# Kernel tuning notes

Hardware: AMD Instinct MI355X
Metric: run time of the kernel (lower is better)

Reference implementation:

```python
import jax, jax.numpy as jnp
import numpy as np

D_IN = 1024
D_OUT = 1024
NUM_HEAD = 16
HEAD_DIM = D_OUT // NUM_HEAD
CTX = 2048


def setup_inputs() -> dict:
    key = jax.random.key(0)
    ks = jax.random.split(key, 7)
    s = 0.02
    x = jax.random.normal(ks[0], (2, CTX, D_IN), dtype=jnp.float32)
    Wq = jax.random.normal(ks[1], (D_IN, D_OUT), dtype=jnp.float32) * s
    Wk = jax.random.normal(ks[2], (D_IN, D_OUT), dtype=jnp.float32) * s
    Wv = jax.random.normal(ks[3], (D_IN, D_OUT), dtype=jnp.float32) * s
    Wo = jax.random.normal(ks[4], (D_OUT, D_OUT), dtype=jnp.float32) * s
    bo = jax.random.normal(ks[5], (D_OUT,), dtype=jnp.float32) * s
    return {"x": x, "Wq": Wq, "Wk": Wk, "Wv": Wv, "Wo": Wo, "bo": bo}


def reference(x, Wq, Wk, Wv, Wo, bo):
    B, T, _ = x.shape
    # QKV projections, split into heads: [B, H, T, hd]
    def split_heads(y):
        return y.reshape(B, T, NUM_HEAD, HEAD_DIM).transpose(0, 2, 1, 3)
    q = split_heads(x @ Wq)
    k = split_heads(x @ Wk)
    v = split_heads(x @ Wv)
    # scaled causal attention scores [B, H, T, T]
    scores = jnp.einsum("bhqd,bhkd->bhqk", q, k) / jnp.sqrt(
        jnp.asarray(HEAD_DIM, dtype=x.dtype))
    causal = jnp.tril(jnp.ones((T, T), dtype=bool))  # mask buffer triu(diag=1) -> keep lower tri
    scores = jnp.where(causal[None, None], scores, jnp.asarray(-jnp.inf, dtype=x.dtype))
    attn = jax.nn.softmax(scores, axis=-1)
    # dropout with droprate=0.0 is identity
    ctx = jnp.einsum("bhqk,bhkd->bhqd", attn, v)
    ctx = ctx.transpose(0, 2, 1, 3).reshape(B, T, D_OUT)
    return ctx @ Wo + bo
```

## Files before the change

kernel.cpp:

```cpp
#include <hip/hip_runtime.h>

typedef __bf16 bf16x8 __attribute__((ext_vector_type(8)));
typedef float f32x4 __attribute__((ext_vector_type(4)));
typedef float f32x16 __attribute__((ext_vector_type(16)));
typedef unsigned int u32x4 __attribute__((ext_vector_type(4)));

__device__ inline unsigned short f2bf(float f) {
    unsigned int x = __builtin_bit_cast(unsigned int, f);
    x += 0x7fff + ((x >> 16) & 1);
    return (unsigned short)(x >> 16);
}

__device__ __forceinline__ void gl_lds16(const unsigned short* g, unsigned short* l)
{
    __builtin_amdgcn_global_load_lds(
        (const __attribute__((address_space(1))) void*)g,
        (__attribute__((address_space(3))) void*)l, 16, 0, 0);
}

__global__ __launch_bounds__(256)
void prep(const float* __restrict__ x, unsigned short* __restrict__ xb,
          const float* __restrict__ Wq, const float* __restrict__ Wk,
          const float* __restrict__ Wv, unsigned short* __restrict__ wT)
{
    __shared__ unsigned short T[64][72];
    if (blockIdx.x < 2048) {
        const size_t i = ((size_t)blockIdx.x * 256 + threadIdx.x) * 8;
        float4 a = *reinterpret_cast<const float4*>(x + i);
        float4 b = *reinterpret_cast<const float4*>(x + i + 4);
        unsigned short t[8] = { f2bf(a.x), f2bf(a.y), f2bf(a.z), f2bf(a.w),
                                f2bf(b.x), f2bf(b.y), f2bf(b.z), f2bf(b.w) };
        *reinterpret_cast<uint4*>(xb + i) = *reinterpret_cast<uint4*>(t);
        return;
    }
    const int blk = blockIdx.x - 2048;
    const int z = blk >> 8, within = blk & 255;
    const float* W = (z == 0) ? Wq : (z == 1) ? Wk : Wv;
    unsigned short* dstBase = wT + (size_t)z * 1024 * 1024;
    const int k0 = (within >> 4) * 64, n0 = (within & 15) * 64;
    const int r = threadIdx.x >> 2, c0 = (threadIdx.x & 3) * 16;
    const float* src = W + (size_t)(k0 + r) * 1024 + n0 + c0;
    #pragma unroll
    for (int j = 0; j < 16; j += 4) {
        float4 f = *reinterpret_cast<const float4*>(src + j);
        T[r][c0 + j]     = f2bf(f.x);
        T[r][c0 + j + 1] = f2bf(f.y);
        T[r][c0 + j + 2] = f2bf(f.z);
        T[r][c0 + j + 3] = f2bf(f.w);
    }
    __syncthreads();
    unsigned short* dst = dstBase + (size_t)(n0 + r) * 1024 + k0 + c0;
    #pragma unroll
    for (int h = 0; h < 2; ++h) {
        unsigned short t8[8];
        #pragma unroll
        for (int j = 0; j < 8; ++j) t8[j] = T[c0 + h * 8 + j][r];
        *reinterpret_cast<uint4*>(dst + h * 8) = *reinterpret_cast<uint4*>(t8);
    }
}

__global__ __launch_bounds__(256)
void wconv(const float* __restrict__ W, unsigned short* __restrict__ wT)
{
    __shared__ unsigned short T[64][72];
    const int k0 = blockIdx.y * 64, n0 = blockIdx.x * 64;
    const int r = threadIdx.x >> 2, c0 = (threadIdx.x & 3) * 16;
    const float* src = W + (size_t)(k0 + r) * 1024 + n0 + c0;
    #pragma unroll
    for (int j = 0; j < 16; j += 4) {
        float4 f = *reinterpret_cast<const float4*>(src + j);
        T[r][c0 + j]     = f2bf(f.x);
        T[r][c0 + j + 1] = f2bf(f.y);
        T[r][c0 + j + 2] = f2bf(f.z);
        T[r][c0 + j + 3] = f2bf(f.w);
    }
    __syncthreads();
    unsigned short* dst = wT + (size_t)(n0 + r) * 1024 + k0 + c0;
    #pragma unroll
    for (int h = 0; h < 2; ++h) {
        unsigned short t8[8];
        #pragma unroll
        for (int j = 0; j < 8; ++j) t8[j] = T[c0 + h * 8 + j][r];
        *reinterpret_cast<uint4*>(dst + h * 8) = *reinterpret_cast<uint4*>(t8);
    }
}

__global__ __launch_bounds__(512, 4)
void gemm8p(const unsigned short* __restrict__ A,
            const unsigned short* __restrict__ BT,
            unsigned short* __restrict__ qb,
            unsigned short* __restrict__ kb,
            unsigned short* __restrict__ vT)
{
    __shared__ unsigned short As[2][128 * 64];
    __shared__ unsigned short Bs[2][192 * 64];

    const int tid  = threadIdx.x;
    const int wave = tid >> 6, lane = tid & 63;
    const int quad = lane >> 4, l16 = lane & 15;
    const int wm = wave >> 2, wn = wave & 3;
    const int mBase = blockIdx.y * 128, nBase = blockIdx.x * 192;

    f32x4 acc[4][3] = {};

    const int arow = tid >> 3;
    const int u8   = (tid & 7) ^ (arow & 7);
    const int rx   = l16 & 7;

    auto stage = [&](int kb0, int buf) {
        #pragma unroll
        for (int i = 0; i < 2; ++i)
            gl_lds16(A + (size_t)(mBase + i * 64 + arow) * 1024 + kb0 + u8 * 8,
                     &As[buf][(i * 512 + wave * 64) * 8]);
        #pragma unroll
        for (int i = 0; i < 3; ++i)
            gl_lds16(BT + (size_t)(nBase + i * 64 + arow) * 1024 + kb0 + u8 * 8,
                     &Bs[buf][(i * 512 + wave * 64) * 8]);
    };

    stage(0, 0);
    __syncthreads();

    for (int t = 0; t < 16; ++t) {
        const int buf = t & 1;
        if (t + 1 < 16)
            stage((t + 1) * 64, buf ^ 1);

        #pragma unroll
        for (int kh = 0; kh < 2; ++kh) {
            bf16x8 af[4], bf[3];
            #pragma unroll
            for (int mr = 0; mr < 4; ++mr) {
                const int row = wm * 64 + mr * 16 + l16;
                af[mr] = *reinterpret_cast<const bf16x8*>(
                    &As[buf][row * 64 + (((kh * 4 + quad) ^ rx) * 8)]);
            }
            #pragma unroll
            for (int nr = 0; nr < 3; ++nr) {
                const int row = wn * 48 + nr * 16 + l16;
                bf[nr] = *reinterpret_cast<const bf16x8*>(
                    &Bs[buf][row * 64 + (((kh * 4 + quad) ^ rx) * 8)]);
            }
            #pragma unroll
            for (int mr = 0; mr < 4; ++mr)
                #pragma unroll
                for (int nr = 0; nr < 3; ++nr)
                    acc[mr][nr] = __builtin_amdgcn_mfma_f32_16x16x32_bf16(
                        af[mr], bf[nr], acc[mr][nr], 0, 0, 0);
        }

        if (t + 1 < 16) {
            asm volatile("s_waitcnt vmcnt(0)" ::: "memory");
            __builtin_amdgcn_s_barrier();
        }
    }

    #pragma unroll
    for (int mr = 0; mr < 4; ++mr) {
        const int row0 = mBase + wm * 64 + mr * 16 + quad * 4;
        #pragma unroll
        for (int nr = 0; nr < 3; ++nr) {
            const int col = nBase + wn * 48 + nr * 16 + l16;
            if (col < 1024) {
                #pragma unroll
                for (int i = 0; i < 4; ++i)
                    qb[(size_t)(row0 + i) * 1024 + col] = f2bf(acc[mr][nr][i]);
            } else if (col < 2048) {
                #pragma unroll
                for (int i = 0; i < 4; ++i)
                    kb[(size_t)(row0 + i) * 1024 + col - 1024] = f2bf(acc[mr][nr][i]);
            } else {
                unsigned short t4[4] = { f2bf(acc[mr][nr][0]), f2bf(acc[mr][nr][1]),
                                         f2bf(acc[mr][nr][2]), f2bf(acc[mr][nr][3]) };
                *reinterpret_cast<uint2*>(&vT[(size_t)(col - 2048) * 4096 + row0]) =
                    *reinterpret_cast<uint2*>(t4);
            }
        }
    }
}

template <int MODE>
__global__ __launch_bounds__(256)
void gemm128(const unsigned short* __restrict__ A,
             const unsigned short* __restrict__ BT,
             void* __restrict__ C0, void* __restrict__ C1,
             void* __restrict__ C2, const float* __restrict__ bias)
{
    __shared__ unsigned short As[128 * 32];
    __shared__ unsigned short Bs[128 * 32];

    const int tid = threadIdx.x;
    const int wave = tid >> 6, lane = tid & 63, quad = lane >> 4, l16 = lane & 15;
    const int wm = wave >> 1, wn = wave & 1;
    const int mBase = blockIdx.y * 128, nBase = blockIdx.x * 128;

    f32x4 acc[4][4] = {};

    const int srow = lane >> 2, sko = (lane & 3) * 8;

    for (int kb = 0; kb < 1024; kb += 32) {
        __syncthreads();
        #pragma unroll
        for (int j = 0; j < 2; ++j) {
            const int seg = wave * 2 + j;
            gl_lds16(A  + (size_t)(mBase + seg * 16 + srow) * 1024 + kb + sko,
                     As + seg * 512);
            gl_lds16(BT + (size_t)(nBase + seg * 16 + srow) * 1024 + kb + sko,
                     Bs + seg * 512);
        }
        __syncthreads();

        bf16x8 af[4], bf[4];
        #pragma unroll
        for (int t = 0; t < 4; ++t) {
            af[t] = *reinterpret_cast<const bf16x8*>(&As[(wm * 64 + t * 16 + l16) * 32 + quad * 8]);
            bf[t] = *reinterpret_cast<const bf16x8*>(&Bs[(wn * 64 + t * 16 + l16) * 32 + quad * 8]);
        }
        #pragma unroll
        for (int ti = 0; ti < 4; ++ti)
            #pragma unroll
            for (int tj = 0; tj < 4; ++tj)
                acc[ti][tj] = __builtin_amdgcn_mfma_f32_16x16x32_bf16(
                    af[ti], bf[tj], acc[ti][tj], 0, 0, 0);
    }

    #pragma unroll
    for (int ti = 0; ti < 4; ++ti) {
        const int row0 = mBase + wm * 64 + ti * 16 + quad * 4;
        #pragma unroll
        for (int tj = 0; tj < 4; ++tj) {
            const int col = nBase + wn * 64 + tj * 16 + l16;
            float* out = (float*)C0;
            const float ba = bias[col];
            #pragma unroll
            for (int i = 0; i < 4; ++i)
                out[(size_t)(row0 + i) * 1024 + col] = acc[ti][tj][i] + ba;
        }
    }
}

__global__ __launch_bounds__(256, 2)
void attn11(const unsigned short* __restrict__ q,
            const unsigned short* __restrict__ k,
            const unsigned short* __restrict__ vT,
            unsigned short* __restrict__ ctx)
{
    __shared__ unsigned short Ks[3][64 * 64];
    __shared__ unsigned short Vs[3][64 * 64];
    __shared__ float Lt[8 * 64];

    const int tid  = threadIdx.x;
    const int wave = tid >> 6, lane = tid & 63;
    const int q32 = lane & 31, hi = lane >> 5;
    const int slice = wave & 1;
    const int ks    = wave >> 1;
    const int j  = blockIdx.x;
    const int bh = blockIdx.y;
    const int b = bh >> 4, h = bh & 15;
    const int tokBase = b * 2048;
    const int colBase = h * 64;
    const int qtA = 31 - j, qtB = j;
    const int qloA = qtA * 64 + slice * 32;
    const int qloB = qtB * 64 + slice * 32;

    bf16x8 aqA[4], aqB[4];
    {
        const unsigned short* ra = q + (size_t)(tokBase + qloA + q32) * 1024 + colBase + hi * 8;
        const unsigned short* rb = q + (size_t)(tokBase + qloB + q32) * 1024 + colBase + hi * 8;
        #pragma unroll
        for (int c = 0; c < 4; ++c) {
            aqA[c] = *reinterpret_cast<const bf16x8*>(ra + c * 16);
            aqB[c] = *reinterpret_cast<const bf16x8*>(rb + c * 16);
        }
    }
    #pragma unroll
    for (int c = 0; c < 4; ++c)
        asm volatile("" :: "v"(aqA[c]), "v"(aqB[c]));

    f32x16 oA[2] = {}, oB[2] = {};
    float lsA = 0.0f, lsB = 0.0f;

    const int s0 = (wave * 2 + 0) * 64 + lane;
    const int s1 = (wave * 2 + 1) * 64 + lane;
    const int r0 = s0 >> 3, sw0 = (s0 & 7) ^ (r0 & 7);
    const int r1 = s1 >> 3, sw1 = (s1 & 7) ^ (r1 & 7);
    const size_t kOff0 = (size_t)r0 * 1024 + colBase + sw0 * 8;
    const size_t kOff1 = (size_t)r1 * 1024 + colBase + sw1 * 8;
    const size_t vOff0 = (size_t)(colBase + r0) * 4096 + sw0 * 8;
    const size_t vOff1 = (size_t)(colBase + r1) * 4096 + sw1 * 8;

    auto stage = [&](int tok0, int buf) {
        gl_lds16(k  + (size_t)tok0 * 1024 + kOff0, &Ks[buf][(wave * 2 + 0) * 512]);
        gl_lds16(k  + (size_t)tok0 * 1024 + kOff1, &Ks[buf][(wave * 2 + 1) * 512]);
        gl_lds16(vT + vOff0 + tok0,                &Vs[buf][(wave * 2 + 0) * 512]);
        gl_lds16(vT + vOff1 + tok0,                &Vs[buf][(wave * 2 + 1) * 512]);
    };

    bf16x8 ak[4];
    bf16x8 bv[2][2];

    const int nkt = qtA + 1;
    stage(tokBase, 0);
    stage(tokBase + 64, 1);

    int cur = 0;
    const int krowK = ks * 32 + q32;
    for (int kt = 0; kt < nkt; ++kt) {
        if (kt + 1 < nkt) asm volatile("s_waitcnt vmcnt(4)" ::: "memory");
        else              asm volatile("s_waitcnt vmcnt(0)" ::: "memory");
        __builtin_amdgcn_s_barrier();
        asm volatile("" ::: "memory");

        const int stg = (cur == 0) ? 2 : cur - 1;
        if (kt + 2 < nkt)
            stage(tokBase + (kt + 2) * 64, stg);

        const unsigned short* KsB = Ks[cur];
        const unsigned short* VsB = Vs[cur];
        #pragma unroll
        for (int c = 0; c < 4; ++c) {
            const int u = c * 2 + hi;
            ak[c] = *reinterpret_cast<const bf16x8*>(
                &KsB[krowK * 64 + ((u ^ (krowK & 7)) * 8)]);
        }
        #pragma unroll
        for (int kc = 0; kc < 2; ++kc)
            #pragma unroll
            for (int dh = 0; dh < 2; ++dh) {
                const int vrow = dh * 32 + q32;
                const int u = ks * 4 + kc * 2 + hi;
                bv[kc][dh] = *reinterpret_cast<const bf16x8*>(
                    &VsB[vrow * 64 + ((u ^ (vrow & 7)) * 8)]);
            }

        const int klo = kt * 64 + ks * 32;
        const bool dB = (klo <= qloB + 31);
        const bool dA = (klo <= qloA + 31);

        if (dB) {
            f32x16 scA = (f32x16)0.0f, scB = (f32x16)0.0f;
            #pragma unroll
            for (int c = 0; c < 4; ++c) {
                scA = __builtin_amdgcn_mfma_f32_32x32x16_bf16(ak[c], aqA[c], scA, 0, 0, 0);
                scB = __builtin_amdgcn_mfma_f32_32x32x16_bf16(ak[c], aqB[c], scB, 0, 0, 0);
            }
            float pA[16], pB[16];
            #pragma unroll
            for (int r = 0; r < 16; ++r) {
                pA[r] = __expf(scA[r] * 0.125f);
                pB[r] = __expf(scB[r] * 0.125f);
            }
            if (klo + 31 > qloB) {
                #pragma unroll
                for (int r = 0; r < 16; ++r) {
                    const int krow = (r & 3) + 8 * (r >> 2) + 4 * hi;
                    if (klo + krow > qloB + q32) pB[r] = 0.0f;
                }
            }
            #pragma unroll
            for (int r = 0; r < 16; ++r) { lsA += pA[r]; lsB += pB[r]; }
            unsigned int pkA[8], pkB[8];
            #pragma unroll
            for (int i = 0; i < 8; ++i) {
                asm("v_cvt_pk_bf16_f32 %0, %1, %2"
                    : "=v"(pkA[i]) : "v"(pA[2 * i]), "v"(pA[2 * i + 1]));
                asm("v_cvt_pk_bf16_f32 %0, %1, %2"
                    : "=v"(pkB[i]) : "v"(pB[2 * i]), "v"(pB[2 * i + 1]));
            }
            #pragma unroll
            for (int kc = 0; kc < 2; ++kc) {
                unsigned int xa0 = pkA[kc * 4 + 0], ya0 = pkA[kc * 4 + 2];
                unsigned int xa1 = pkA[kc * 4 + 1], ya1 = pkA[kc * 4 + 3];
                unsigned int xb0 = pkB[kc * 4 + 0], yb0 = pkB[kc * 4 + 2];
                unsigned int xb1 = pkB[kc * 4 + 1], yb1 = pkB[kc * 4 + 3];
                asm("v_permlane32_swap_b32 %0, %1" : "+v"(xa0), "+v"(ya0));
                asm("v_permlane32_swap_b32 %0, %1" : "+v"(xa1), "+v"(ya1));
                asm("v_permlane32_swap_b32 %0, %1" : "+v"(xb0), "+v"(yb0));
                asm("v_permlane32_swap_b32 %0, %1" : "+v"(xb1), "+v"(yb1));
                const u32x4 wa = { xa0, xa1, ya0, ya1 };
                const u32x4 wb = { xb0, xb1, yb0, yb1 };
                const bf16x8 paA = __builtin_bit_cast(bf16x8, wa);
                const bf16x8 paB = __builtin_bit_cast(bf16x8, wb);
                #pragma unroll
                for (int dh = 0; dh < 2; ++dh) {
                    oA[dh] = __builtin_amdgcn_mfma_f32_32x32x16_bf16(paA, bv[kc][dh], oA[dh], 0, 0, 0);
                    oB[dh] = __builtin_amdgcn_mfma_f32_32x32x16_bf16(paB, bv[kc][dh], oB[dh], 0, 0, 0);
                }
            }
        } else if (dA) {
            f32x16 sc = (f32x16)0.0f;
            #pragma unroll
            for (int c = 0; c < 4; ++c)
                sc = __builtin_amdgcn_mfma_f32_32x32x16_bf16(ak[c], aqA[c], sc, 0, 0, 0);
            float p[16];
            #pragma unroll
            for (int r = 0; r < 16; ++r) p[r] = __expf(sc[r] * 0.125f);
            if (klo + 31 > qloA) {
                #pragma unroll
                for (int r = 0; r < 16; ++r) {
                    const int krow = (r & 3) + 8 * (r >> 2) + 4 * hi;
                    if (klo + krow > qloA + q32) p[r] = 0.0f;
                }
            }
            #pragma unroll
            for (int r = 0; r < 16; ++r) lsA += p[r];
            unsigned int pk[8];
            #pragma unroll
            for (int i = 0; i < 8; ++i)
                asm("v_cvt_pk_bf16_f32 %0, %1, %2"
                    : "=v"(pk[i]) : "v"(p[2 * i]), "v"(p[2 * i + 1]));
            #pragma unroll
            for (int kc = 0; kc < 2; ++kc) {
                unsigned int x0 = pk[kc * 4 + 0], y0 = pk[kc * 4 + 2];
                unsigned int x1 = pk[kc * 4 + 1], y1 = pk[kc * 4 + 3];
                asm("v_permlane32_swap_b32 %0, %1" : "+v"(x0), "+v"(y0));
                asm("v_permlane32_swap_b32 %0, %1" : "+v"(x1), "+v"(y1));
                const u32x4 wv = { x0, x1, y0, y1 };
                const bf16x8 pa = __builtin_bit_cast(bf16x8, wv);
                #pragma unroll
                for (int dh = 0; dh < 2; ++dh)
                    oA[dh] = __builtin_amdgcn_mfma_f32_32x32x16_bf16(pa, bv[kc][dh], oA[dh], 0, 0, 0);
            }
        }
        cur = (cur == 2) ? 0 : cur + 1;
    }

    float* Obuf = reinterpret_cast<float*>(&Ks[0][0]);

    __syncthreads();
    Lt[(wave * 2 + 0) * 64 + lane] = lsA;
    Lt[(wave * 2 + 1) * 64 + lane] = lsB;

    auto writePartial = [&](const f32x16 (&o)[2]) {
        float* slot = Obuf + slice * 2048;
        #pragma unroll
        for (int r = 0; r < 16; ++r) {
            const int row = (r & 3) + 8 * (r >> 2) + 4 * hi;
            #pragma unroll
            for (int dh = 0; dh < 2; ++dh)
                slot[row * 64 + dh * 32 + q32] = o[dh][r];
        }
    };
    auto finalize = [&](int t, int qt, const f32x16 (&o)[2]) {
        const float lf = Lt[(slice * 2 + t) * 64 + q32]
                       + Lt[(slice * 2 + t) * 64 + 32 + q32]
                       + Lt[((slice + 2) * 2 + t) * 64 + q32]
                       + Lt[((slice + 2) * 2 + t) * 64 + 32 + q32];
        const float inv = 1.0f / lf;
        const float* slot = Obuf + slice * 2048;
        #pragma unroll
        for (int r = 0; r < 16; ++r) {
            const int row = (r & 3) + 8 * (r >> 2) + 4 * hi;
            const float invr = __shfl(inv, row);
            const size_t gr = (size_t)(tokBase + qt * 64 + slice * 32 + row) * 1024 + colBase;
            #pragma unroll
            for (int dh = 0; dh < 2; ++dh)
                ctx[gr + dh * 32 + q32] =
                    f2bf((o[dh][r] + slot[row * 64 + dh * 32 + q32]) * invr);
        }
    };

    if (ks == 1) writePartial(oA);
    __syncthreads();
    if (ks == 0) finalize(0, qtA, oA);
    __syncthreads();
    if (ks == 0) writePartial(oB);
    __syncthreads();
    if (ks == 1) finalize(1, qtB, oB);
}

extern "C" void kernel_launch(void* const* d_in, const int* in_sizes, int n_in,
                              void* d_out, int out_size, void* d_ws, size_t ws_size,
                              hipStream_t stream)
{
    const float* x  = (const float*)d_in[0];
    const float* Wq = (const float*)d_in[1];
    const float* Wk = (const float*)d_in[2];
    const float* Wv = (const float*)d_in[3];
    const float* Wo = (const float*)d_in[4];
    const float* bo = (const float*)d_in[5];
    float* out = (float*)d_out;

    unsigned short* xb     = (unsigned short*)d_ws;
    unsigned short* qb     = xb + (size_t)4096 * 1024;
    unsigned short* kb     = qb + (size_t)4096 * 1024;
    unsigned short* vT     = kb + (size_t)4096 * 1024;
    unsigned short* ctx    = xb;
    unsigned short* wqkvT  = (unsigned short*)d_out;
    unsigned short* woT    = kb;

    prep<<<2816, 256, 0, stream>>>(x, xb, Wq, Wk, Wv, wqkvT);

    gemm8p<<<dim3(16, 32), 512, 0, stream>>>(xb, wqkvT, qb, kb, vT);

    attn11<<<dim3(16, 32), 256, 0, stream>>>(qb, kb, vT, ctx);

    wconv<<<dim3(16, 16), 256, 0, stream>>>(Wo, woT);

    gemm128<2><<<dim3(8, 32), 256, 0, stream>>>(ctx, woT, out, nullptr, nullptr, bo);
}
```

Measured before the change: 179.3 us.

## Fuse Wo bf16 conversion into output GEMM with double-buffered K-64 pipeline

Removes the separate wconv kernel. The output-projection GEMM now reads fp32 Wo directly, converts it to bf16 and transposes it into padded LDS as it goes. The GEMM also moves from K=32 single-buffered steps to K=64 double-buffered tiles, with an XOR-swizzled A layout and the next tile's global loads overlapped with MFMA work. The aim is to save a kernel launch and the Wo round trip through global memory, and to cut barrier overhead. The cost is that each of the 32 row blocks now converts Wo again, and register and LDS pressure go up.

```diff
diff --git a/kernel.cpp b/kernel.cpp
--- a/kernel.cpp
+++ b/kernel.cpp
@@ -59,32 +59,6 @@
     }
 }
 
-__global__ __launch_bounds__(256)
-void wconv(const float* __restrict__ W, unsigned short* __restrict__ wT)
-{
-    __shared__ unsigned short T[64][72];
-    const int k0 = blockIdx.y * 64, n0 = blockIdx.x * 64;
-    const int r = threadIdx.x >> 2, c0 = (threadIdx.x & 3) * 16;
-    const float* src = W + (size_t)(k0 + r) * 1024 + n0 + c0;
-    #pragma unroll
-    for (int j = 0; j < 16; j += 4) {
-        float4 f = *reinterpret_cast<const float4*>(src + j);
-        T[r][c0 + j]     = f2bf(f.x);
-        T[r][c0 + j + 1] = f2bf(f.y);
-        T[r][c0 + j + 2] = f2bf(f.z);
-        T[r][c0 + j + 3] = f2bf(f.w);
-    }
-    __syncthreads();
-    unsigned short* dst = wT + (size_t)(n0 + r) * 1024 + k0 + c0;
-    #pragma unroll
-    for (int h = 0; h < 2; ++h) {
-        unsigned short t8[8];
-        #pragma unroll
-        for (int j = 0; j < 8; ++j) t8[j] = T[c0 + h * 8 + j][r];
-        *reinterpret_cast<uint4*>(dst + h * 8) = *reinterpret_cast<uint4*>(t8);
-    }
-}
-
 __global__ __launch_bounds__(512, 4)
 void gemm8p(const unsigned short* __restrict__ A,
             const unsigned short* __restrict__ BT,
@@ -179,15 +153,14 @@
     }
 }
 
-template <int MODE>
-__global__ __launch_bounds__(256)
-void gemm128(const unsigned short* __restrict__ A,
-             const unsigned short* __restrict__ BT,
-             void* __restrict__ C0, void* __restrict__ C1,
-             void* __restrict__ C2, const float* __restrict__ bias)
+__global__ __launch_bounds__(256, 2)
+void gemm2f(const unsigned short* __restrict__ A,
+            const float* __restrict__ Wo,
+            float* __restrict__ out,
+            const float* __restrict__ bias)
 {
-    __shared__ unsigned short As[128 * 32];
-    __shared__ unsigned short Bs[128 * 32];
+    __shared__ unsigned short As[2][128 * 64];
+    __shared__ unsigned short Bs[2][128 * 72];
 
     const int tid = threadIdx.x;
     const int wave = tid >> 6, lane = tid & 63, quad = lane >> 4, l16 = lane & 15;
@@ -196,45 +169,90 @@
 
     f32x4 acc[4][4] = {};
 
-    const int srow = lane >> 2, sko = (lane & 3) * 8;
-
-    for (int kb = 0; kb < 1024; kb += 32) {
-        __syncthreads();
-        #pragma unroll
-        for (int j = 0; j < 2; ++j) {
-            const int seg = wave * 2 + j;
-            gl_lds16(A  + (size_t)(mBase + seg * 16 + srow) * 1024 + kb + sko,
-                     As + seg * 512);
-            gl_lds16(BT + (size_t)(nBase + seg * 16 + srow) * 1024 + kb + sko,
-                     Bs + seg * 512);
-        }
-        __syncthreads();
-
-        bf16x8 af[4], bf[4];
-        #pragma unroll
-        for (int t = 0; t < 4; ++t) {
-            af[t] = *reinterpret_cast<const bf16x8*>(&As[(wm * 64 + t * 16 + l16) * 32 + quad * 8]);
-            bf[t] = *reinterpret_cast<const bf16x8*>(&Bs[(wn * 64 + t * 16 + l16) * 32 + quad * 8]);
-        }
-        #pragma unroll
-        for (int ti = 0; ti < 4; ++ti)
-            #pragma unroll
-            for (int tj = 0; tj < 4; ++tj)
-                acc[ti][tj] = __builtin_amdgcn_mfma_f32_16x16x32_bf16(
-                    af[ti], bf[tj], acc[ti][tj], 0, 0, 0);
+    const int arow = tid >> 3;
+    const int u8   = (tid & 7) ^ (arow & 7);
+    const int rx   = l16 & 7;
+
+    auto stageA = [&](int kb0, int buf) {
+        #pragma unroll
+        for (int i = 0; i < 4; ++i)
+            gl_lds16(A + (size_t)(mBase + i * 32 + arow) * 1024 + kb0 + u8 * 8,
+                     &As[buf][(i * 256 + tid) * 8]);
+    };
+
+    const int kr = tid >> 2;
+    const int c0 = (tid & 3) * 4;
+    float4 breg[8];
+
+    auto loadB = [&](int kb0) {
+        #pragma unroll
+        for (int j = 0; j < 8; ++j)
+            breg[j] = *reinterpret_cast<const float4*>(
+                &Wo[(size_t)(kb0 + kr) * 1024 + nBase + c0 + j * 16]);
+    };
+    auto writeB = [&](int buf) {
+        #pragma unroll
+        for (int j = 0; j < 8; ++j) {
+            const int c = c0 + j * 16;
+            Bs[buf][(c + 0) * 72 + kr] = f2bf(breg[j].x);
+            Bs[buf][(c + 1) * 72 + kr] = f2bf(breg[j].y);
+            Bs[buf][(c + 2) * 72 + kr] = f2bf(breg[j].z);
+            Bs[buf][(c + 3) * 72 + kr] = f2bf(breg[j].w);
+        }
+    };
+
+    loadB(0);
+    stageA(0, 0);
+    writeB(0);
+    __syncthreads();
+
+    for (int t = 0; t < 16; ++t) {
+        const int buf = t & 1;
+        if (t + 1 < 16) {
+            stageA((t + 1) * 64, buf ^ 1);
+            loadB((t + 1) * 64);
+        }
+
+        #pragma unroll
+        for (int kh = 0; kh < 2; ++kh) {
+            bf16x8 af[4], bf[4];
+            #pragma unroll
+            for (int mr = 0; mr < 4; ++mr) {
+                const int row = wm * 64 + mr * 16 + l16;
+                af[mr] = *reinterpret_cast<const bf16x8*>(
+                    &As[buf][row * 64 + (((kh * 4 + quad) ^ rx) * 8)]);
+            }
+            #pragma unroll
+            for (int nr = 0; nr < 4; ++nr) {
+                const int row = wn * 64 + nr * 16 + l16;
+                bf[nr] = *reinterpret_cast<const bf16x8*>(
+                    &Bs[buf][row * 72 + kh * 32 + quad * 8]);
+            }
+            #pragma unroll
+            for (int mr = 0; mr < 4; ++mr)
+                #pragma unroll
+                for (int nr = 0; nr < 4; ++nr)
+                    acc[mr][nr] = __builtin_amdgcn_mfma_f32_16x16x32_bf16(
+                        af[mr], bf[nr], acc[mr][nr], 0, 0, 0);
+        }
+
+        if (t + 1 < 16) {
+            writeB(buf ^ 1);
+            asm volatile("s_waitcnt vmcnt(0) lgkmcnt(0)" ::: "memory");
+            __builtin_amdgcn_s_barrier();
+        }
     }
 
     #pragma unroll
-    for (int ti = 0; ti < 4; ++ti) {
-        const int row0 = mBase + wm * 64 + ti * 16 + quad * 4;
-        #pragma unroll
-        for (int tj = 0; tj < 4; ++tj) {
-            const int col = nBase + wn * 64 + tj * 16 + l16;
-            float* out = (float*)C0;
+    for (int mr = 0; mr < 4; ++mr) {
+        const int row0 = mBase + wm * 64 + mr * 16 + quad * 4;
+        #pragma unroll
+        for (int nr = 0; nr < 4; ++nr) {
+            const int col = nBase + wn * 64 + nr * 16 + l16;
             const float ba = bias[col];
             #pragma unroll
             for (int i = 0; i < 4; ++i)
-                out[(size_t)(row0 + i) * 1024 + col] = acc[ti][tj][i] + ba;
+                out[(size_t)(row0 + i) * 1024 + col] = acc[mr][nr][i] + ba;
         }
     }
 }
@@ -487,7 +505,6 @@
     unsigned short* vT     = kb + (size_t)4096 * 1024;
     unsigned short* ctx    = xb;
     unsigned short* wqkvT  = (unsigned short*)d_out;
-    unsigned short* woT    = kb;
 
     prep<<<2816, 256, 0, stream>>>(x, xb, Wq, Wk, Wv, wqkvT);
 
@@ -495,7 +512,5 @@
 
     attn11<<<dim3(16, 32), 256, 0, stream>>>(qb, kb, vT, ctx);
 
-    wconv<<<dim3(16, 16), 256, 0, stream>>>(Wo, woT);
-
-    gemm128<2><<<dim3(8, 32), 256, 0, stream>>>(ctx, woT, out, nullptr, nullptr, bo);
-}
+    gemm2f<<<dim3(8, 32), 256, 0, stream>>>(ctx, Wo, out, bo);
+}
```

New measurement: 187.3 us. 1.04x slower.
